# Kernel optimization log

Hardware: AMD Instinct MI355X
Metric: run time of the kernel (lower is better)

The kernel has to match this reference:

```python
import jax, jax.numpy as jnp
import numpy as np
import math

B, S, H = 2, 2048, 2048
NH, HD = 32, 64
BASE, SCALE = 10000.0, 2.0
MAX_POS, ORIG_MAX_POS = 8192, 8192
BETA_FAST, BETA_SLOW = 32, 1
EPS = 1e-6


def _yarn_cos_sin():
    # revised_yarn: scale inv_freq by 1/((1-mask)*scale + mask)
    inv_freq = 1.0 / BASE ** (np.arange(0, HD, 2, dtype=np.float64) / HD)
    def corr(nr):
        return HD * math.log(ORIG_MAX_POS / (nr * 2 * math.pi)) / (2 * math.log(BASE))
    low = max(math.floor(corr(BETA_FAST)), 0)
    high = min(math.ceil(corr(BETA_SLOW)), HD - 1)
    hi = high + 0.001 if low == high else high
    ramp = np.clip((np.arange(HD // 2, dtype=np.float64) - low) / (hi - low), 0.0, 1.0)
    mask = 1.0 - ramp  # extrapolation_factor = 1
    inv_freq = inv_freq / ((1.0 - mask) * SCALE + mask)
    mscale = (0.1 * math.log(SCALE) + 1.0) if SCALE > 1 else 1.0
    t = np.arange(MAX_POS, dtype=np.float64)
    freqs = np.outer(t, inv_freq)
    emb = np.concatenate([freqs, freqs], axis=-1)
    return np.cos(emb) * mscale, np.sin(emb) * mscale

_COS_NP, _SIN_NP = _yarn_cos_sin()


def rotate_half(x):
    x1, x2 = jnp.split(x, 2, axis=-1)
    return jnp.concatenate([-x2, x1], axis=-1)


def rms_norm(x, w):
    v = jnp.mean(jnp.square(x.astype(jnp.float32)), axis=-1, keepdims=True)
    return (x.astype(jnp.float32) * jax.lax.rsqrt(v + EPS)).astype(x.dtype) * w


def localized_filtering(x, lf1, lf2, w1, b1, w2, b2, ln_w):
    # x: (B,S,H); torch works in (B,H,S,1) with kernel-(2,1) convs over seq
    residual = x
    xi = jnp.transpose(x, (0, 2, 1))[:, :, :, None]  # (B,H,S,1)
    xi = jnp.concatenate([lf1, xi], axis=2)          # (B,H,S+1,1)
    dn = ('NCHW', 'OIHW', 'NCHW')
    o1 = jax.lax.conv_general_dilated(xi, w1, (1, 1), 'VALID', dimension_numbers=dn)
    o1 = o1 + b1[None, :, None, None]                # (B,H/2,S,1)
    o1c = jnp.concatenate([lf2, o1], axis=2)         # (B,H/2,S+1,1)
    o2 = jax.lax.conv_general_dilated(o1c, w2, (1, 1), 'VALID', dimension_numbers=dn)
    o2 = o2 + b2[None, :, None, None]                # (B,H,S,1)
    o2 = jnp.transpose(o2[:, :, :, 0], (0, 2, 1))    # (B,S,H)
    return rms_norm(o2 + residual, ln_w)


def setup_inputs():
    key = jax.random.key(0)
    ks = jax.random.split(key, 8)
    f = lambda k, shp: jax.random.normal(k, shp, dtype=jnp.float32) * 0.02
    return {
        'hidden_states': jax.random.normal(ks[0], (B, S, H), dtype=jnp.float32),
        'position_ids': jnp.broadcast_to(jnp.arange(S, dtype=jnp.int32)[None, :], (B, S)),
        'lf1_cache': jnp.zeros((B, H, 1, 1), jnp.float32),
        'lf2_cache': jnp.zeros((B, H // 2, 1, 1), jnp.float32),
        'Wqk': f(ks[1], (2 * H, H)),
        'Wv': f(ks[2], (H, H)),
        'Wo': f(ks[3], (H, H)),
        'conv1_w': f(ks[4], (H // 2, H, 2, 1)),
        'conv1_b': jnp.zeros((H // 2,), jnp.float32),
        'conv2_w': f(ks[5], (H, H // 2, 2, 1)),
        'conv2_b': jnp.zeros((H,), jnp.float32),
        'ln_w': jnp.ones((H,), jnp.float32),
    }


def reference(hidden_states, position_ids, lf1_cache, lf2_cache, Wqk, Wv, Wo,
              conv1_w, conv1_b, conv2_w, conv2_b, ln_w):
    cos = jnp.asarray(_COS_NP, jnp.float32)
    sin = jnp.asarray(_SIN_NP, jnp.float32)
    # v from raw hidden states
    v = (hidden_states @ Wv.T).reshape(B, S, NH, HD).transpose(0, 2, 1, 3)  # (B,NH,S,HD)
    # localized filtering gate feeds q/k projection
    lf = localized_filtering(hidden_states, lf1_cache, lf2_cache,
                             conv1_w, conv1_b, conv2_w, conv2_b, ln_w)
    qk = (lf @ Wqk.T).reshape(B, S, NH, 2 * HD)  # per-head [q|k] split
    q = qk[..., :HD].transpose(0, 2, 1, 3)       # (B,NH,S,HD)
    k = qk[..., HD:].transpose(0, 2, 1, 3)
    cos_p = cos[position_ids][:, None, :, :]     # (B,1,S,HD)
    sin_p = sin[position_ids][:, None, :, :]
    q = q * cos_p + rotate_half(q) * sin_p
    k = k * cos_p + rotate_half(k) * sin_p
    scores = jnp.einsum('bhqd,bhkd->bhqk', q, k) / math.sqrt(HD)
    causal = jnp.tril(jnp.ones((S, S), dtype=bool))
    scores = jnp.where(causal[None, None], scores, jnp.finfo(scores.dtype).min)
    attn = jax.nn.softmax(scores, axis=-1)
    ctx = jnp.einsum('bhqk,bhkd->bhqd', attn, v)
    out = ctx.transpose(0, 2, 1, 3).reshape(B, S, H) @ Wo.T
    return out
```

## Files before the change

### kernel.cpp

```cpp
#include <hip/hip_runtime.h>
#include <hip/hip_bf16.h>
#include <math.h>
#include <stdint.h>

typedef __hip_bfloat16 bf16;
using f32x4 = __attribute__((ext_vector_type(4))) float;
using s16x8 = __attribute__((ext_vector_type(8))) short;

constexpr int Bc = 2, Sc = 2048, Hc = 2048, NHc = 32, HDc = 64;
constexpr int Mc = Bc * Sc;
constexpr int MAXPOS = 8192;

constexpr size_t OFF_WV  = 0;
constexpr size_t OFF_WQK = OFF_WV  + (size_t)Hc * Hc * 2;
constexpr size_t OFF_WO  = OFF_WQK + (size_t)2 * Hc * Hc * 2;
constexpr size_t OFF_W1  = OFF_WO  + (size_t)Hc * Hc * 2;
constexpr size_t OFF_W2  = OFF_W1  + (size_t)(Hc/2) * (2*Hc) * 2;
constexpr size_t OFF_HS  = OFF_W2  + (size_t)Hc * Hc * 2;
constexpr size_t OFF_XPR = OFF_HS  + (size_t)Mc * Hc * 2;
constexpr size_t OFF_O1  = OFF_XPR + (size_t)Mc * Hc * 2;
constexpr size_t OFF_O1P = OFF_O1  + (size_t)Mc * (Hc/2) * 2;
constexpr size_t OFF_O2  = OFF_O1P + (size_t)Mc * (Hc/2) * 2;
constexpr size_t OFF_LF  = OFF_O2  + (size_t)Mc * Hc * 4;
constexpr size_t OFF_VT  = OFF_LF  + (size_t)Mc * Hc * 2;
constexpr size_t OFF_COS = OFF_VT  + (size_t)Mc * Hc * 2;
constexpr size_t OFF_SIN = OFF_COS + (size_t)MAXPOS * HDc * 4;
constexpr size_t OFF_QK  = OFF_O2;
constexpr size_t OFF_Q   = OFF_XPR;
constexpr size_t OFF_K   = OFF_HS;
constexpr size_t OFF_CTX = OFF_O1;

__device__ __forceinline__ f32x4 mfma16(s16x8 a, s16x8 b, f32x4 c) {
  return __builtin_amdgcn_mfma_f32_16x16x32_bf16(a, b, c, 0, 0, 0);
}
__device__ __forceinline__ void gload16(const bf16* g, bf16* l) {
  __builtin_amdgcn_global_load_lds(
      (__attribute__((address_space(1))) void*)g,
      (__attribute__((address_space(3))) void*)l, 16, 0, 0);
}
__device__ __forceinline__ uint16_t bfbits(float x) {
  union { bf16 h; uint16_t u; } v; v.h = __float2bfloat16(x); return v.u;
}
__device__ __forceinline__ uint32_t pkbf(float a, float b) {
  return (uint32_t)bfbits(a) | ((uint32_t)bfbits(b) << 16);
}
__device__ __forceinline__ void block_bar() {
  asm volatile("" ::: "memory");
  __builtin_amdgcn_s_barrier();
  asm volatile("" ::: "memory");
}
template <int N> __device__ __forceinline__ void vm_wait() {
  if constexpr (N == 0)      asm volatile("s_waitcnt vmcnt(0)" ::: "memory");
  else if constexpr (N == 3) asm volatile("s_waitcnt vmcnt(3)" ::: "memory");
  else if constexpr (N == 4) asm volatile("s_waitcnt vmcnt(4)" ::: "memory");
  else if constexpr (N == 6) asm volatile("s_waitcnt vmcnt(6)" ::: "memory");
  else if constexpr (N == 8) asm volatile("s_waitcnt vmcnt(8)" ::: "memory");
}

__global__ void k_cvt(const float* __restrict__ in, bf16* __restrict__ out, int n) {
  int i = blockIdx.x * 256 + threadIdx.x;
  if (i < n) out[i] = __float2bfloat16(in[i]);
}

__global__ void k_cvt_hs(const float* __restrict__ hs, const float* __restrict__ lf1,
                         bf16* __restrict__ hsb, bf16* __restrict__ xprev) {
  int i = blockIdx.x * 256 + threadIdx.x;
  if (i >= Mc * Hc) return;
  float v = hs[i];
  bf16 b = __float2bfloat16(v);
  hsb[i] = b;
  int row = i >> 11, col = i & (Hc - 1);
  int s = row & (Sc - 1), bb = row >> 11;
  if (s + 1 < Sc) xprev[i + Hc] = b;
  if (s == 0)     xprev[i] = __float2bfloat16(lf1[bb * Hc + col]);
}

__global__ void k_repack1(const float* __restrict__ w, bf16* __restrict__ out) {
  int i = blockIdx.x * 256 + threadIdx.x;
  if (i >= (Hc/2) * 2 * Hc) return;
  int oc = i >> 12, k = i & 4095;
  int ic = k & (Hc - 1), t = k >> 11;
  out[i] = __float2bfloat16(w[((size_t)oc * Hc + ic) * 2 + t]);
}
__global__ void k_repack2(const float* __restrict__ w, bf16* __restrict__ out) {
  int i = blockIdx.x * 256 + threadIdx.x;
  if (i >= Hc * Hc) return;
  int c = i >> 11, k = i & (Hc - 1);
  int oc = k & (Hc/2 - 1), t = k >> 10;
  out[i] = __float2bfloat16(w[((size_t)c * (Hc/2) + oc) * 2 + t]);
}

__global__ void k_prefill_o1p(const float* __restrict__ lf2, bf16* __restrict__ o1p) {
  int i = blockIdx.x * 256 + threadIdx.x;
  if (i >= Bc * (Hc/2)) return;
  int b = i >> 10, n = i & (Hc/2 - 1);
  o1p[(size_t)b * Sc * (Hc/2) + n] = __float2bfloat16(lf2[i]);
}

struct InvF { double v[32]; double mscale; };

__global__ void k_costab(InvF f, float* __restrict__ ct, float* __restrict__ st) {
  int i = blockIdx.x * 256 + threadIdx.x;
  if (i >= MAXPOS * HDc) return;
  int p = i >> 6, d = i & 63;
  double ang = (double)p * f.v[d & 31];
  ct[i] = (float)(cos(ang) * f.mscale);
  st[i] = (float)(sin(ang) * f.mscale);
}

__global__ __launch_bounds__(256) void k_rmsnorm(const float* __restrict__ x,
                                                 const float* __restrict__ w,
                                                 bf16* __restrict__ out) {
  __shared__ float red[4];
  int row = blockIdx.x;
  const float* xr = x + (size_t)row * Hc;
  float ss = 0.f;
  for (int c = threadIdx.x; c < Hc; c += 256) { float v = xr[c]; ss += v * v; }
  for (int off = 32; off; off >>= 1) ss += __shfl_down(ss, off, 64);
  if ((threadIdx.x & 63) == 0) red[threadIdx.x >> 6] = ss;
  __syncthreads();
  float sc = rsqrtf((red[0] + red[1] + red[2] + red[3]) / Hc + 1e-6f);
  for (int c = threadIdx.x; c < Hc; c += 256)
    out[(size_t)row * Hc + c] = __float2bfloat16(xr[c] * sc * w[c]);
}

__global__ void k_rope(const bf16* __restrict__ qk, const int* __restrict__ pos,
                       const float* __restrict__ ct, const float* __restrict__ st,
                       bf16* __restrict__ qo, bf16* __restrict__ ko) {
  const float QSC = 0.125f * 1.44269504088896f;
  int i = blockIdx.x * 256 + threadIdx.x;
  if (i >= Mc * NHc * 32) return;
  int d = i & 31, h = (i >> 5) & 31, row = i >> 10;
  int p = pos[row];
  float c0 = ct[p * 64 + d],      s0 = st[p * 64 + d];
  float c1 = ct[p * 64 + 32 + d], s1 = st[p * 64 + 32 + d];
  const bf16* base = qk + (size_t)row * 4096 + h * 128;
  float q0 = __bfloat162float(base[d]),      q1 = __bfloat162float(base[d + 32]);
  float k0 = __bfloat162float(base[64 + d]), k1 = __bfloat162float(base[96 + d]);
  int b = row >> 11, s = row & (Sc - 1);
  size_t o = ((size_t)(b * NHc + h) * Sc + s) * 64 + d;
  qo[o]      = __float2bfloat16((q0 * c0 - q1 * s0) * QSC);
  qo[o + 32] = __float2bfloat16((q1 * c1 + q0 * s1) * QSC);
  ko[o]      = __float2bfloat16(k0 * c0 - k1 * s0);
  ko[o + 32] = __float2bfloat16(k1 * c1 + k0 * s1);
}

template <int EPI, int BM = 128>
__global__ __launch_bounds__(256) void gemm_bt(
    const bf16* __restrict__ A0, const bf16* __restrict__ A1, int Ksplit,
    const bf16* __restrict__ Bw, int K, int N, void* __restrict__ Cout,
    const float* __restrict__ bias, const float* __restrict__ resid,
    bf16* __restrict__ aux) {
  constexpr int MR = BM / 32;
  __shared__ __align__(16) bf16 As[2][BM * 32];
  __shared__ __align__(16) bf16 Bs[2][128 * 32];
  const int tid = threadIdx.x;
  const int bm = blockIdx.y, bn = blockIdx.x;
  const int w = tid >> 6, l = tid & 63;
  const int wm = (w >> 1) * (BM / 2), wn = (w & 1) * 64;
  const int lrow = l & 15, lg = l >> 4, lk = lg * 8;
  const int r0 = tid >> 2, cofs = (tid & 3) * 8;

  auto stage = [&](int buf, int kt) {
    const int kcol = kt * 32;
    const bf16* Au; int kc;
    if (kcol < Ksplit) { Au = A0; kc = kcol; } else { Au = A1; kc = kcol - Ksplit; }
    gload16(Au + (size_t)(bm * BM + r0) * Ksplit + kc + cofs,        &As[buf][tid * 8]);
    if constexpr (BM == 128)
      gload16(Au + (size_t)(bm * BM + r0 + 64) * Ksplit + kc + cofs, &As[buf][2048 + tid * 8]);
    gload16(Bw + (size_t)(bn * 128 + r0) * K + kcol + cofs,          &Bs[buf][tid * 8]);
    gload16(Bw + (size_t)(bn * 128 + r0 + 64) * K + kcol + cofs,     &Bs[buf][2048 + tid * 8]);
  };

  f32x4 acc[MR][4] = {};
  const int nkt = K / 32;
  stage(0, 0);
  __syncthreads();
  for (int kt = 0; kt < nkt; ++kt) {
    const int cur = kt & 1;
    if (kt + 1 < nkt) stage(cur ^ 1, kt + 1);
    s16x8 af[MR], bfr[4];
#pragma unroll
    for (int m = 0; m < MR; ++m)
      af[m] = *(const s16x8*)&As[cur][(wm + m * 16 + lrow) * 32 + lk];
#pragma unroll
    for (int n = 0; n < 4; ++n)
      bfr[n] = *(const s16x8*)&Bs[cur][(wn + n * 16 + lrow) * 32 + lk];
    __builtin_amdgcn_s_setprio(1);
#pragma unroll
    for (int m = 0; m < MR; ++m)
#pragma unroll
      for (int n = 0; n < 4; ++n)
        acc[m][n] = mfma16(af[m], bfr[n], acc[m][n]);
    __builtin_amdgcn_s_setprio(0);
    __syncthreads();
  }
#pragma unroll
  for (int m = 0; m < MR; ++m)
#pragma unroll
    for (int n = 0; n < 4; ++n)
#pragma unroll
      for (int r = 0; r < 4; ++r) {
        const int grow = bm * BM + wm + m * 16 + lg * 4 + r;
        const int gcol = bn * 128 + wn + n * 16 + lrow;
        float v = acc[m][n][r];
        if constexpr (EPI == 1) {
          v += bias[gcol];
          bf16 bv = __float2bfloat16(v);
          ((bf16*)Cout)[(size_t)grow * N + gcol] = bv;
          if ((grow & (Sc - 1)) != Sc - 1) aux[(size_t)(grow + 1) * N + gcol] = bv;
        } else {
          ((float*)Cout)[(size_t)grow * N + gcol] = v;
        }
      }
}

template <int EPI, int BN>
__global__ __launch_bounds__(512, 2) void gemm8(
    const bf16* __restrict__ A0, const bf16* __restrict__ A1, int Ksplit,
    const bf16* __restrict__ Bw, int K, int N, void* __restrict__ Cout,
    const float* __restrict__ bias, const float* __restrict__ resid) {
  constexpr int BM = 256;
  constexpr int L = (BN == 256) ? 4 : 3;
  constexpr int TILE = (BM + BN) * 32;
  constexpr int MR = (BN == 256) ? 8 : 4;
  __shared__ __align__(16) bf16 lds[3][TILE];
  const int tid = threadIdx.x;
  const int w = tid >> 6, l = tid & 63;
  const int lrow = l & 15, lg = l >> 4;
  const int wm = (BN == 256) ? (w >> 2) * 128 : (w & 3) * 64;
  const int wn = (BN == 256) ? (w & 3) * 64 : (w >> 2) * 64;
  const int gx = gridDim.x;
  const int lin = blockIdx.y * gx + blockIdx.x;
  const int cx = gx >> 2, cy = gridDim.y >> 1;
  const int c = lin & 7, idx = lin >> 3;
  const int bn = (c & 3) * cx + idx % cx;
  const int bm = (c >> 2) * cy + idx / cx;

  auto ld1 = [&](const bf16* srcbase, size_t stride, bf16* ldst, int ci) {
    const int pr = ci >> 3, rem = ci & 7;
    const int r = pr * 2 + (rem >> 2), g = (rem & 3) ^ (pr & 3);
    gload16(srcbase + (size_t)r * stride + g * 8, ldst + ci * 8);
  };
  auto stage = [&](int kt, int slot) {
    const int kcol = kt * 32;
    const bf16* Au; int kc;
    if (kcol < Ksplit) { Au = A0; kc = kcol; } else { Au = A1; kc = kcol - Ksplit; }
    const bf16* As_ = Au + (size_t)bm * BM * Ksplit + kc;
    bf16* ldsA = lds[slot];
    ld1(As_, Ksplit, ldsA, tid);
    ld1(As_, Ksplit, ldsA, tid + 512);
    const bf16* Bs_ = Bw + (size_t)bn * BN * K + kcol;
    bf16* ldsB = lds[slot] + BM * 32;
    ld1(Bs_, K, ldsB, tid);
    if constexpr (BN == 256) ld1(Bs_, K, ldsB, tid + 512);
  };
  auto frag = [&](const bf16* base, int r) -> s16x8 {
    const int s = ((r >> 1) << 3) + ((r & 1) << 2) + (lg ^ ((r >> 1) & 3));
    return *(const s16x8*)(base + s * 8);
  };

  f32x4 acc[MR][4] = {};
  const int nkt = K / 32;
  stage(0, 0);
  stage(1, 1);
  for (int t = 0; t < nkt; ++t) {
    if (t + 2 < nkt) { stage(t + 2, (t + 2) % 3); vm_wait<2 * L>(); }
    else if (t + 1 < nkt) { vm_wait<L>(); }
    else { vm_wait<0>(); }
    block_bar();
    const bf16* Asl = lds[t % 3];
    const bf16* Bsl = Asl + BM * 32;
    s16x8 af[MR], bfr[4];
#pragma unroll
    for (int m = 0; m < MR; ++m) af[m] = frag(Asl, wm + m * 16 + lrow);
#pragma unroll
    for (int n = 0; n < 4; ++n) bfr[n] = frag(Bsl, wn + n * 16 + lrow);
    __builtin_amdgcn_s_setprio(1);
#pragma unroll
    for (int m = 0; m < MR; ++m)
#pragma unroll
      for (int n = 0; n < 4; ++n)
        acc[m][n] = mfma16(af[m], bfr[n], acc[m][n]);
    __builtin_amdgcn_s_setprio(0);
    block_bar();
  }
#pragma unroll
  for (int m = 0; m < MR; ++m)
#pragma unroll
    for (int n = 0; n < 4; ++n)
#pragma unroll
      for (int r = 0; r < 4; ++r) {
        const int grow = bm * BM + wm + m * 16 + lg * 4 + r;
        const int gcol = bn * BN + wn + n * 16 + lrow;
        float v = acc[m][n][r];
        if constexpr (EPI == 0) {
          ((bf16*)Cout)[(size_t)grow * N + gcol] = __float2bfloat16(v);
        } else if constexpr (EPI == 2) {
          v += bias[gcol] + resid[(size_t)grow * N + gcol];
          ((float*)Cout)[(size_t)grow * N + gcol] = v;
        } else if constexpr (EPI == 5) {
          const int b = gcol >> 11, s = gcol & (Sc - 1);
          ((bf16*)Cout)[((size_t)(b * Hc + grow)) * Sc + s] = __float2bfloat16(v);
        } else {
          ((float*)Cout)[(size_t)grow * N + gcol] = v;
        }
      }
}

__global__ __launch_bounds__(256) void k_attn(const bf16* __restrict__ Q,
                                              const bf16* __restrict__ Kg,
                                              const bf16* __restrict__ Vt,
                                              bf16* __restrict__ ctx) {
  __shared__ __align__(16) bf16 Ks[2][64 * 64];
  __shared__ __align__(16) bf16 Vs[2][64 * 64];
  __shared__ __align__(16) uint32_t Pl[4][2][2][16][20];
  const int tid = threadIdx.x;
  const int w = tid >> 6, l = tid & 63;
  const int lrow = l & 15, lg = l >> 4, lk = lg * 8;
  const int bh = blockIdx.x;
  const int tile = blockIdx.y;
  const bf16* Qp = Q  + (size_t)bh * Sc * HDc;
  const bf16* Kp = Kg + (size_t)bh * Sc * HDc;
  const bf16* Vp = Vt + (size_t)bh * HDc * Sc;
  const int b = bh >> 5, h = bh & 31;
  const s16x8 ones8 = {16256, 16256, 16256, 16256, 16256, 16256, 16256, 16256};

  const int srow0 = tid >> 3, schunk = tid & 7;

  for (int pass = 0; pass < 2; ++pass) {
    const int base = (pass == 0) ? tile * 128 : (Sc - 128 - tile * 128);
    const int q0 = base + w * 32;
    const int NT = base / 64 + 2;

    s16x8 qa[2][2];
#pragma unroll
    for (int m = 0; m < 2; ++m)
#pragma unroll
      for (int hf = 0; hf < 2; ++hf)
        qa[m][hf] = *(const s16x8*)&Qp[(size_t)(q0 + m * 16 + lrow) * 64 + hf * 32 + lk];

    f32x4 o[2][4] = {};
    f32x4 lsf[2] = {};
    float mx[2] = {-1e30f, -1e30f};

    {
      gload16(Kp + (size_t)srow0 * 64 + ((schunk ^ (srow0 & 7)) << 3), &Ks[0][tid * 8]);
      gload16(Kp + (size_t)(32 + srow0) * 64 + ((schunk ^ ((32 + srow0) & 7)) << 3),
              &Ks[0][2048 + tid * 8]);
      gload16(Vp + (size_t)srow0 * Sc + ((schunk ^ (srow0 & 7)) << 3), &Vs[0][tid * 8]);
      gload16(Vp + (size_t)(32 + srow0) * Sc + ((schunk ^ ((32 + srow0) & 7)) << 3),
              &Vs[0][2048 + tid * 8]);
    }
    __syncthreads();

    for (int t = 0; t < NT; ++t) {
      const int cur = t & 1;
      const int kv0 = t * 64;
      if (t + 1 < NT) {
        const int nkv = kv0 + 64;
        const int nb = cur ^ 1;
        gload16(Kp + (size_t)(nkv + srow0) * 64 + ((schunk ^ (srow0 & 7)) << 3),
                &Ks[nb][tid * 8]);
        gload16(Kp + (size_t)(nkv + 32 + srow0) * 64 + ((schunk ^ ((32 + srow0) & 7)) << 3),
                &Ks[nb][2048 + tid * 8]);
        gload16(Vp + (size_t)srow0 * Sc + nkv + ((schunk ^ (srow0 & 7)) << 3),
                &Vs[nb][tid * 8]);
        gload16(Vp + (size_t)(32 + srow0) * Sc + nkv + ((schunk ^ ((32 + srow0) & 7)) << 3),
                &Vs[nb][2048 + tid * 8]);
      }
      if (kv0 <= q0) {
        s16x8 kc[8], vc[4][2];
#pragma unroll
        for (int c = 0; c < 4; ++c)
#pragma unroll
          for (int hf = 0; hf < 2; ++hf) {
            const int row = c * 16 + lrow;
            kc[c * 2 + hf] =
                *(const s16x8*)&Ks[cur][row * 64 + (((hf << 2) + lg) ^ (row & 7)) * 8];
          }
#pragma unroll
        for (int db = 0; db < 4; ++db)
#pragma unroll
          for (int kh = 0; kh < 2; ++kh) {
            const int row = db * 16 + lrow;
            vc[db][kh] =
                *(const s16x8*)&Vs[cur][row * 64 + (((kh << 2) + lg) ^ (row & 7)) * 8];
          }
        const bool lastit = (kv0 + 64 > q0);

#pragma unroll
        for (int m = 0; m < 2; ++m) {
          f32x4 s[4];
          __builtin_amdgcn_s_setprio(1);
#pragma unroll
          for (int c = 0; c < 4; ++c) {
            f32x4 z = {};
            z = mfma16(kc[c * 2], qa[m][0], z);
            z = mfma16(kc[c * 2 + 1], qa[m][1], z);
            s[c] = z;
          }
          __builtin_amdgcn_s_setprio(0);

          if (lastit) {
            const int qq = q0 + m * 16 + lrow;
#pragma unroll
            for (int c = 0; c < 4; ++c)
#pragma unroll
              for (int r = 0; r < 4; ++r)
                if (kv0 + c * 16 + lg * 4 + r > qq) s[c][r] = -1e30f;
          }
          float t16 = fmaxf(
              fmaxf(fmaxf(fmaxf(s[0][0], s[0][1]), fmaxf(s[0][2], s[0][3])),
                    fmaxf(fmaxf(s[1][0], s[1][1]), fmaxf(s[1][2], s[1][3]))),
              fmaxf(fmaxf(fmaxf(s[2][0], s[2][1]), fmaxf(s[2][2], s[2][3])),
                    fmaxf(fmaxf(s[3][0], s[3][1]), fmaxf(s[3][2], s[3][3]))));
          if (!__all(t16 <= mx[m] + 8.0f)) {
            t16 = fmaxf(t16, __shfl_xor(t16, 16, 64));
            t16 = fmaxf(t16, __shfl_xor(t16, 32, 64));
            const float mnew = fmaxf(mx[m], t16);
            const float sold = __builtin_amdgcn_exp2f(mx[m] - mnew);
            mx[m] = mnew;
            lsf[m] *= sold;
#pragma unroll
            for (int db = 0; db < 4; ++db) o[m][db] *= sold;
          }
          float p[4][4];
#pragma unroll
          for (int c = 0; c < 4; ++c)
#pragma unroll
            for (int r = 0; r < 4; ++r)
              p[c][r] = __builtin_amdgcn_exp2f(s[c][r] - mx[m]);
#pragma unroll
          for (int kh = 0; kh < 2; ++kh) {
            *(uint64_t*)&Pl[w][m][kh][lrow][lg * 2] =
                (uint64_t)pkbf(p[kh * 2][0], p[kh * 2][1]) |
                ((uint64_t)pkbf(p[kh * 2][2], p[kh * 2][3]) << 32);
            *(uint64_t*)&Pl[w][m][kh][lrow][8 + lg * 2] =
                (uint64_t)pkbf(p[kh * 2 + 1][0], p[kh * 2 + 1][1]) |
                ((uint64_t)pkbf(p[kh * 2 + 1][2], p[kh * 2 + 1][3]) << 32);
          }
          const s16x8 pb0 = *(const s16x8*)&Pl[w][m][0][lrow][lg * 4];
          const s16x8 pb1 = *(const s16x8*)&Pl[w][m][1][lrow][lg * 4];
          __builtin_amdgcn_s_setprio(1);
#pragma unroll
          for (int db = 0; db < 4; ++db) o[m][db] = mfma16(vc[db][0], pb0, o[m][db]);
          lsf[m] = mfma16(ones8, pb0, lsf[m]);
#pragma unroll
          for (int db = 0; db < 4; ++db) o[m][db] = mfma16(vc[db][1], pb1, o[m][db]);
          lsf[m] = mfma16(ones8, pb1, lsf[m]);
          __builtin_amdgcn_s_setprio(0);
        }
      }
      __syncthreads();
    }
#pragma unroll
    for (int m = 0; m < 2; ++m) {
      const float inv = 1.0f / lsf[m][0];
      const int qrow = q0 + m * 16 + lrow;
      const size_t rowoff = ((size_t)(b * Sc + qrow)) * Hc + h * 64;
#pragma unroll
      for (int db = 0; db < 4; ++db) {
        uint64_t pk = (uint64_t)bfbits(o[m][db][0] * inv) |
                      ((uint64_t)bfbits(o[m][db][1] * inv) << 16) |
                      ((uint64_t)bfbits(o[m][db][2] * inv) << 32) |
                      ((uint64_t)bfbits(o[m][db][3] * inv) << 48);
        *(uint64_t*)&ctx[rowoff + db * 16 + lg * 4] = pk;
      }
    }
    __syncthreads();
  }
}

extern "C" void kernel_launch(void* const* d_in, const int* in_sizes, int n_in,
                              void* d_out, int out_size, void* d_ws, size_t ws_size,
                              hipStream_t stream) {
  (void)in_sizes; (void)n_in; (void)out_size; (void)ws_size;
  const float* hs  = (const float*)d_in[0];
  const int*   pos = (const int*)d_in[1];
  const float* lf1 = (const float*)d_in[2];
  const float* lf2 = (const float*)d_in[3];
  const float* Wqk = (const float*)d_in[4];
  const float* Wv  = (const float*)d_in[5];
  const float* Wo  = (const float*)d_in[6];
  const float* c1w = (const float*)d_in[7];
  const float* c1b = (const float*)d_in[8];
  const float* c2w = (const float*)d_in[9];
  const float* c2b = (const float*)d_in[10];
  const float* lnw = (const float*)d_in[11];
  float* out = (float*)d_out;
  char*  ws  = (char*)d_ws;

  bf16* wvB   = (bf16*)(ws + OFF_WV);
  bf16* wqkB  = (bf16*)(ws + OFF_WQK);
  bf16* woB   = (bf16*)(ws + OFF_WO);
  bf16* w1B   = (bf16*)(ws + OFF_W1);
  bf16* w2B   = (bf16*)(ws + OFF_W2);
  bf16* hsB   = (bf16*)(ws + OFF_HS);
  bf16* xprB  = (bf16*)(ws + OFF_XPR);
  bf16* o1B   = (bf16*)(ws + OFF_O1);
  bf16* o1pB  = (bf16*)(ws + OFF_O1P);
  float* o2F  = (float*)(ws + OFF_O2);
  bf16* lfB   = (bf16*)(ws + OFF_LF);
  bf16* vtB   = (bf16*)(ws + OFF_VT);
  float* cosT = (float*)(ws + OFF_COS);
  float* sinT = (float*)(ws + OFF_SIN);
  bf16* qkB   = (bf16*)(ws + OFF_QK);
  bf16* qB    = (bf16*)(ws + OFF_Q);
  bf16* kB    = (bf16*)(ws + OFF_K);
  bf16* ctxB  = (bf16*)(ws + OFF_CTX);

  InvF f;
  {
    const double base = 10000.0, scale = 2.0;
    const int hd = HDc;
    auto corr = [&](double nr) {
      return hd * log(8192.0 / (nr * 2.0 * M_PI)) / (2.0 * log(base));
    };
    double low = floor(corr(32.0)); if (low < 0) low = 0;
    double high = ceil(corr(1.0));  if (high > hd - 1) high = hd - 1;
    double hi = (low == high) ? high + 0.001 : high;
    for (int i = 0; i < 32; ++i) {
      double inv = 1.0 / pow(base, (2.0 * i) / hd);
      double ramp = ((double)i - low) / (hi - low);
      ramp = ramp < 0.0 ? 0.0 : (ramp > 1.0 ? 1.0 : ramp);
      double mask = 1.0 - ramp;
      f.v[i] = inv / ((1.0 - mask) * scale + mask);
    }
    f.mscale = 0.1 * log(scale) + 1.0;
  }

  k_cvt<<<(Hc * Hc + 255) / 256, 256, 0, stream>>>(Wv, wvB, Hc * Hc);
  k_cvt<<<(2 * Hc * Hc + 255) / 256, 256, 0, stream>>>(Wqk, wqkB, 2 * Hc * Hc);
  k_cvt<<<(Hc * Hc + 255) / 256, 256, 0, stream>>>(Wo, woB, Hc * Hc);
  k_repack1<<<((Hc / 2) * 2 * Hc + 255) / 256, 256, 0, stream>>>(c1w, w1B);
  k_repack2<<<(Hc * Hc + 255) / 256, 256, 0, stream>>>(c2w, w2B);
  k_cvt_hs<<<(Mc * Hc + 255) / 256, 256, 0, stream>>>(hs, lf1, hsB, xprB);
  k_prefill_o1p<<<(Bc * (Hc / 2) + 255) / 256, 256, 0, stream>>>(lf2, o1pB);
  k_costab<<<(MAXPOS * HDc + 255) / 256, 256, 0, stream>>>(f, cosT, sinT);

  gemm_bt<1, 64><<<dim3((Hc / 2) / 128, Mc / 64), 256, 0, stream>>>(
      xprB, hsB, Hc, w1B, 2 * Hc, Hc / 2, o1B, c1b, nullptr, o1pB);
  gemm8<5, 128><<<dim3(Mc / 128, Hc / 256), 512, 0, stream>>>(
      wvB, wvB, Hc, hsB, Hc, Mc, vtB, nullptr, nullptr);
  gemm8<2, 128><<<dim3(Hc / 128, Mc / 256), 512, 0, stream>>>(
      o1pB, o1B, Hc / 2, w2B, Hc, Hc, o2F, c2b, hs);
  k_rmsnorm<<<Mc, 256, 0, stream>>>(o2F, lnw, lfB);
  gemm8<0, 256><<<dim3((2 * Hc) / 256, Mc / 256), 512, 0, stream>>>(
      lfB, lfB, Hc, wqkB, Hc, 2 * Hc, qkB, nullptr, nullptr);
  k_rope<<<(Mc * NHc * 32 + 255) / 256, 256, 0, stream>>>(qkB, pos, cosT, sinT, qB, kB);
  k_attn<<<dim3(64, 8), 256, 0, stream>>>(qB, kB, vtB, ctxB);
  gemm8<4, 128><<<dim3(Hc / 128, Mc / 256), 512, 0, stream>>>(
      ctxB, ctxB, Hc, woB, Hc, Hc, out, nullptr, nullptr);
}
```

Measured before the change: 472.9 us.

## Fuse RoPE into QK projection GEMM epilogue and triple-buffer attention K/V loads

The QK projection GEMM now applies the rotary embedding and Q scaling in its epilogue and writes Q and K directly in head-major layout. This removes the separate RoPE kernel and the round trip of the intermediate QK buffer through memory. Separately, the attention kernel moves from double- to triple-buffered K/V staging with counted vmem waits, so loads are issued two tiles ahead. The GEMM epilogue gains extra cos/sin table reads and scattered bf16 stores, and the attention kernel uses more LDS.

Result: slower. 503.9 us (+6.6%).

```diff
diff --git a/kernel.cpp b/kernel.cpp
--- a/kernel.cpp
+++ b/kernel.cpp
@@ -25,7 +25,6 @@
 constexpr size_t OFF_VT  = OFF_LF  + (size_t)Mc * Hc * 2;
 constexpr size_t OFF_COS = OFF_VT  + (size_t)Mc * Hc * 2;
 constexpr size_t OFF_SIN = OFF_COS + (size_t)MAXPOS * HDc * 4;
-constexpr size_t OFF_QK  = OFF_O2;
 constexpr size_t OFF_Q   = OFF_XPR;
 constexpr size_t OFF_K   = OFF_HS;
 constexpr size_t OFF_CTX = OFF_O1;
@@ -122,27 +121,6 @@
   float sc = rsqrtf((red[0] + red[1] + red[2] + red[3]) / Hc + 1e-6f);
   for (int c = threadIdx.x; c < Hc; c += 256)
     out[(size_t)row * Hc + c] = __float2bfloat16(xr[c] * sc * w[c]);
-}
-
-__global__ void k_rope(const bf16* __restrict__ qk, const int* __restrict__ pos,
-                       const float* __restrict__ ct, const float* __restrict__ st,
-                       bf16* __restrict__ qo, bf16* __restrict__ ko) {
-  const float QSC = 0.125f * 1.44269504088896f;
-  int i = blockIdx.x * 256 + threadIdx.x;
-  if (i >= Mc * NHc * 32) return;
-  int d = i & 31, h = (i >> 5) & 31, row = i >> 10;
-  int p = pos[row];
-  float c0 = ct[p * 64 + d],      s0 = st[p * 64 + d];
-  float c1 = ct[p * 64 + 32 + d], s1 = st[p * 64 + 32 + d];
-  const bf16* base = qk + (size_t)row * 4096 + h * 128;
-  float q0 = __bfloat162float(base[d]),      q1 = __bfloat162float(base[d + 32]);
-  float k0 = __bfloat162float(base[64 + d]), k1 = __bfloat162float(base[96 + d]);
-  int b = row >> 11, s = row & (Sc - 1);
-  size_t o = ((size_t)(b * NHc + h) * Sc + s) * 64 + d;
-  qo[o]      = __float2bfloat16((q0 * c0 - q1 * s0) * QSC);
-  qo[o + 32] = __float2bfloat16((q1 * c1 + q0 * s1) * QSC);
-  ko[o]      = __float2bfloat16(k0 * c0 - k1 * s0);
-  ko[o + 32] = __float2bfloat16(k1 * c1 + k0 * s1);
 }
 
 template <int EPI, int BM = 128>
@@ -219,7 +197,9 @@
 __global__ __launch_bounds__(512, 2) void gemm8(
     const bf16* __restrict__ A0, const bf16* __restrict__ A1, int Ksplit,
     const bf16* __restrict__ Bw, int K, int N, void* __restrict__ Cout,
-    const float* __restrict__ bias, const float* __restrict__ resid) {
+    const float* __restrict__ bias, const float* __restrict__ resid,
+    const int* __restrict__ pos, const float* __restrict__ ct,
+    const float* __restrict__ st, bf16* __restrict__ out2) {
   constexpr int BM = 256;
   constexpr int L = (BN == 256) ? 4 : 3;
   constexpr int TILE = (BM + BN) * 32;
@@ -285,35 +265,58 @@
     __builtin_amdgcn_s_setprio(0);
     block_bar();
   }
-#pragma unroll
-  for (int m = 0; m < MR; ++m)
-#pragma unroll
-    for (int n = 0; n < 4; ++n)
+  if constexpr (EPI == 6) {
+    const int gcol0 = bn * BN + wn;
+    const int h = gcol0 >> 7, half = (gcol0 >> 6) & 1;
+    bf16* outp = half ? out2 : (bf16*)Cout;
+    const float qsc = half ? 1.0f : 0.125f * 1.44269504088896f;
+#pragma unroll
+    for (int m = 0; m < MR; ++m)
 #pragma unroll
       for (int r = 0; r < 4; ++r) {
         const int grow = bm * BM + wm + m * 16 + lg * 4 + r;
-        const int gcol = bn * BN + wn + n * 16 + lrow;
-        float v = acc[m][n][r];
-        if constexpr (EPI == 0) {
-          ((bf16*)Cout)[(size_t)grow * N + gcol] = __float2bfloat16(v);
-        } else if constexpr (EPI == 2) {
-          v += bias[gcol] + resid[(size_t)grow * N + gcol];
-          ((float*)Cout)[(size_t)grow * N + gcol] = v;
-        } else if constexpr (EPI == 5) {
-          const int b = gcol >> 11, s = gcol & (Sc - 1);
-          ((bf16*)Cout)[((size_t)(b * Hc + grow)) * Sc + s] = __float2bfloat16(v);
-        } else {
-          ((float*)Cout)[(size_t)grow * N + gcol] = v;
+        const int p = pos[grow];
+        const int bb = grow >> 11, s = grow & (Sc - 1);
+        bf16* rowp = outp + ((size_t)(bb * NHc + h) * Sc + s) * 64;
+#pragma unroll
+        for (int n = 0; n < 2; ++n) {
+          const int dd = n * 16 + lrow;
+          const float c0 = ct[p * 64 + dd],      s0 = st[p * 64 + dd];
+          const float c1 = ct[p * 64 + 32 + dd], s1 = st[p * 64 + 32 + dd];
+          const float v0 = acc[m][n][r], v1 = acc[m][n + 2][r];
+          rowp[dd]      = __float2bfloat16((v0 * c0 - v1 * s0) * qsc);
+          rowp[dd + 32] = __float2bfloat16((v1 * c1 + v0 * s1) * qsc);
         }
       }
+  } else {
+#pragma unroll
+    for (int m = 0; m < MR; ++m)
+#pragma unroll
+      for (int n = 0; n < 4; ++n)
+#pragma unroll
+        for (int r = 0; r < 4; ++r) {
+          const int grow = bm * BM + wm + m * 16 + lg * 4 + r;
+          const int gcol = bn * BN + wn + n * 16 + lrow;
+          float v = acc[m][n][r];
+          if constexpr (EPI == 2) {
+            v += bias[gcol] + resid[(size_t)grow * N + gcol];
+            ((float*)Cout)[(size_t)grow * N + gcol] = v;
+          } else if constexpr (EPI == 5) {
+            const int b = gcol >> 11, s = gcol & (Sc - 1);
+            ((bf16*)Cout)[((size_t)(b * Hc + grow)) * Sc + s] = __float2bfloat16(v);
+          } else {
+            ((float*)Cout)[(size_t)grow * N + gcol] = v;
+          }
+        }
+  }
 }
 
 __global__ __launch_bounds__(256) void k_attn(const bf16* __restrict__ Q,
                                               const bf16* __restrict__ Kg,
                                               const bf16* __restrict__ Vt,
                                               bf16* __restrict__ ctx) {
-  __shared__ __align__(16) bf16 Ks[2][64 * 64];
-  __shared__ __align__(16) bf16 Vs[2][64 * 64];
+  __shared__ __align__(16) bf16 Ks[3][64 * 64];
+  __shared__ __align__(16) bf16 Vs[3][64 * 64];
   __shared__ __align__(16) uint32_t Pl[4][2][2][16][20];
   const int tid = threadIdx.x;
   const int w = tid >> 6, l = tid & 63;
@@ -328,6 +331,17 @@
 
   const int srow0 = tid >> 3, schunk = tid & 7;
 
+  auto stage = [&](int kv0, int slot) {
+    gload16(Kp + (size_t)(kv0 + srow0) * 64 + ((schunk ^ (srow0 & 7)) << 3),
+            &Ks[slot][tid * 8]);
+    gload16(Kp + (size_t)(kv0 + 32 + srow0) * 64 + ((schunk ^ ((32 + srow0) & 7)) << 3),
+            &Ks[slot][2048 + tid * 8]);
+    gload16(Vp + (size_t)srow0 * Sc + kv0 + ((schunk ^ (srow0 & 7)) << 3),
+            &Vs[slot][tid * 8]);
+    gload16(Vp + (size_t)(32 + srow0) * Sc + kv0 + ((schunk ^ ((32 + srow0) & 7)) << 3),
+            &Vs[slot][2048 + tid * 8]);
+  };
+
   for (int pass = 0; pass < 2; ++pass) {
     const int base = (pass == 0) ? tile * 128 : (Sc - 128 - tile * 128);
     const int q0 = base + w * 32;
@@ -344,32 +358,18 @@
     f32x4 lsf[2] = {};
     float mx[2] = {-1e30f, -1e30f};
 
-    {
-      gload16(Kp + (size_t)srow0 * 64 + ((schunk ^ (srow0 & 7)) << 3), &Ks[0][tid * 8]);
-      gload16(Kp + (size_t)(32 + srow0) * 64 + ((schunk ^ ((32 + srow0) & 7)) << 3),
-              &Ks[0][2048 + tid * 8]);
-      gload16(Vp + (size_t)srow0 * Sc + ((schunk ^ (srow0 & 7)) << 3), &Vs[0][tid * 8]);
-      gload16(Vp + (size_t)(32 + srow0) * Sc + ((schunk ^ ((32 + srow0) & 7)) << 3),
-              &Vs[0][2048 + tid * 8]);
-    }
-    __syncthreads();
+    stage(0, 0);
+    stage(64, 1);
 
     for (int t = 0; t < NT; ++t) {
-      const int cur = t & 1;
       const int kv0 = t * 64;
-      if (t + 1 < NT) {
-        const int nkv = kv0 + 64;
-        const int nb = cur ^ 1;
-        gload16(Kp + (size_t)(nkv + srow0) * 64 + ((schunk ^ (srow0 & 7)) << 3),
-                &Ks[nb][tid * 8]);
-        gload16(Kp + (size_t)(nkv + 32 + srow0) * 64 + ((schunk ^ ((32 + srow0) & 7)) << 3),
-                &Ks[nb][2048 + tid * 8]);
-        gload16(Vp + (size_t)srow0 * Sc + nkv + ((schunk ^ (srow0 & 7)) << 3),
-                &Vs[nb][tid * 8]);
-        gload16(Vp + (size_t)(32 + srow0) * Sc + nkv + ((schunk ^ ((32 + srow0) & 7)) << 3),
-                &Vs[nb][2048 + tid * 8]);
-      }
+      if (t + 2 < NT)      { stage(kv0 + 128, (t + 2) % 3); vm_wait<8>(); }
+      else if (t + 1 < NT) { vm_wait<4>(); }
+      else                 { vm_wait<0>(); }
+      block_bar();
       if (kv0 <= q0) {
+        const bf16* Kc = Ks[t % 3];
+        const bf16* Vc = Vs[t % 3];
         s16x8 kc[8], vc[4][2];
 #pragma unroll
         for (int c = 0; c < 4; ++c)
@@ -377,7 +377,7 @@
           for (int hf = 0; hf < 2; ++hf) {
             const int row = c * 16 + lrow;
             kc[c * 2 + hf] =
-                *(const s16x8*)&Ks[cur][row * 64 + (((hf << 2) + lg) ^ (row & 7)) * 8];
+                *(const s16x8*)&Kc[row * 64 + (((hf << 2) + lg) ^ (row & 7)) * 8];
           }
 #pragma unroll
         for (int db = 0; db < 4; ++db)
@@ -385,7 +385,7 @@
           for (int kh = 0; kh < 2; ++kh) {
             const int row = db * 16 + lrow;
             vc[db][kh] =
-                *(const s16x8*)&Vs[cur][row * 64 + (((kh << 2) + lg) ^ (row & 7)) * 8];
+                *(const s16x8*)&Vc[row * 64 + (((kh << 2) + lg) ^ (row & 7)) * 8];
           }
         const bool lastit = (kv0 + 64 > q0);
 
@@ -452,7 +452,7 @@
           __builtin_amdgcn_s_setprio(0);
         }
       }
-      __syncthreads();
+      block_bar();
     }
 #pragma unroll
     for (int m = 0; m < 2; ++m) {
@@ -468,7 +468,8 @@
         *(uint64_t*)&ctx[rowoff + db * 16 + lg * 4] = pk;
       }
     }
-    __syncthreads();
+    vm_wait<0>();
+    block_bar();
   }
 }
 
@@ -505,7 +506,6 @@
   bf16* vtB   = (bf16*)(ws + OFF_VT);
   float* cosT = (float*)(ws + OFF_COS);
   float* sinT = (float*)(ws + OFF_SIN);
-  bf16* qkB   = (bf16*)(ws + OFF_QK);
   bf16* qB    = (bf16*)(ws + OFF_Q);
   bf16* kB    = (bf16*)(ws + OFF_K);
   bf16* ctxB  = (bf16*)(ws + OFF_CTX);
@@ -542,14 +542,13 @@
   gemm_bt<1, 64><<<dim3((Hc / 2) / 128, Mc / 64), 256, 0, stream>>>(
       xprB, hsB, Hc, w1B, 2 * Hc, Hc / 2, o1B, c1b, nullptr, o1pB);
   gemm8<5, 128><<<dim3(Mc / 128, Hc / 256), 512, 0, stream>>>(
-      wvB, wvB, Hc, hsB, Hc, Mc, vtB, nullptr, nullptr);
+      wvB, wvB, Hc, hsB, Hc, Mc, vtB, nullptr, nullptr, nullptr, nullptr, nullptr, nullptr);
   gemm8<2, 128><<<dim3(Hc / 128, Mc / 256), 512, 0, stream>>>(
-      o1pB, o1B, Hc / 2, w2B, Hc, Hc, o2F, c2b, hs);
+      o1pB, o1B, Hc / 2, w2B, Hc, Hc, o2F, c2b, hs, nullptr, nullptr, nullptr, nullptr);
   k_rmsnorm<<<Mc, 256, 0, stream>>>(o2F, lnw, lfB);
-  gemm8<0, 256><<<dim3((2 * Hc) / 256, Mc / 256), 512, 0, stream>>>(
-      lfB, lfB, Hc, wqkB, Hc, 2 * Hc, qkB, nullptr, nullptr);
-  k_rope<<<(Mc * NHc * 32 + 255) / 256, 256, 0, stream>>>(qkB, pos, cosT, sinT, qB, kB);
+  gemm8<6, 256><<<dim3((2 * Hc) / 256, Mc / 256), 512, 0, stream>>>(
+      lfB, lfB, Hc, wqkB, Hc, 2 * Hc, qB, nullptr, nullptr, pos, cosT, sinT, kB);
   k_attn<<<dim3(64, 8), 256, 0, stream>>>(qB, kB, vtB, ctxB);
   gemm8<4, 128><<<dim3(Hc / 128, Mc / 256), 512, 0, stream>>>(
-      ctxB, ctxB, Hc, woB, Hc, Hc, out, nullptr, nullptr);
-}
+      ctxB, ctxB, Hc, woB, Hc, Hc, out, nullptr, nullptr, nullptr, nullptr, nullptr, nullptr);
+}
```
